# Performance work log

Hardware: AMD Instinct MI355X
Metric: run time of the kernel (lower is better)

The kernel has to match this reference:

```python
import jax, jax.numpy as jnp
import numpy as np

B, S, D = 2, 2048, 1024
H = 16
DH = D // H
FF = 4096
N_NEU = 4096
N_PAT = 64
K = 16          # neuron top-k
KP = 8          # pattern top-k
EPS = 1e-5


def _layer_norm(x, g, b):
    mu = jnp.mean(x, axis=-1, keepdims=True)
    var = jnp.mean((x - mu) ** 2, axis=-1, keepdims=True)
    return (x - mu) * jax.lax.rsqrt(var + EPS) * g + b


def setup_inputs() -> dict:
    key = jax.random.key(0)
    ks = jax.random.split(key, 20)
    sc = 0.02
    lin = lambda k, o, i: jax.random.normal(k, (o, i), jnp.float32) * (1.0 / np.sqrt(i))
    return {
        "x": jax.random.normal(ks[0], (B, S, D), jnp.float32),
        "neurons": jax.random.normal(ks[1], (N_NEU, D), jnp.float32) * sc,
        "wq": lin(ks[2], D, D), "bq": jnp.zeros((D,), jnp.float32),
        "wk": lin(ks[3], D, D), "bk": jnp.zeros((D,), jnp.float32),
        "wv": lin(ks[4], D, D), "bv": jnp.zeros((D,), jnp.float32),
        "wp": lin(ks[5], 2, 2 * D), "bp": jnp.zeros((2,), jnp.float32),
        "pattern_queries": jax.random.normal(ks[6], (N_PAT, D), jnp.float32) * sc,
        "gates": jax.random.normal(ks[7], (N_PAT, FF), jnp.float32) * sc,
        "w_up": lin(ks[8], FF, D), "b_up": jnp.zeros((FF,), jnp.float32),
        "w_down": lin(ks[9], D, FF), "b_down": jnp.zeros((D,), jnp.float32),
        "ln1_g": jnp.ones((D,), jnp.float32), "ln1_b": jnp.zeros((D,), jnp.float32),
        "ln2_g": jnp.ones((D,), jnp.float32), "ln2_b": jnp.zeros((D,), jnp.float32),
    }


def _forward(x, neurons, wq, bq, wk, bk, wv, bv, wp, bp, pattern_queries, gates,
             w_up, b_up, w_down, b_down, ln1_g, ln1_b, ln2_g, ln2_b):
    # ---- NeuronRouter on norm1(x) ----
    normed = _layer_norm(x, ln1_g, ln1_b)
    q = (normed @ wq.T + bq).reshape(B, S, H, DH).transpose(0, 2, 1, 3)
    k = (normed @ wk.T + bk).reshape(B, S, H, DH).transpose(0, 2, 1, 3)
    v = (normed @ wv.T + bv).reshape(B, S, H, DH).transpose(0, 2, 1, 3)
    attn = jax.nn.softmax(jnp.einsum('bhqd,bhkd->bhqk', q, k) / np.sqrt(DH), axis=-1)
    context = jnp.einsum('bhqk,bhkd->bhqd', attn, v).transpose(0, 2, 1, 3).reshape(B, S, D)

    token_scores = normed @ neurons.T                     # [B,S,N]
    context_scores = context @ neurons.T                  # [B,S,N]
    combined = jnp.concatenate([normed, context], axis=-1)
    path_w = jax.nn.softmax(combined @ wp.T + bp, axis=-1)  # [B,S,2]
    scores = path_w[..., 0:1] * token_scores + path_w[..., 1:2] * context_scores

    topk_scores, topk_idx = jax.lax.top_k(scores, K)      # [B,S,K]
    topk_weights = jax.nn.softmax(topk_scores, axis=-1)
    selected = neurons[topk_idx]                          # [B,S,K,D]
    router_out = jnp.einsum('bsk,bskd->bsd', topk_weights, selected)

    x = x + router_out

    # ---- PatternFFN on norm2(x) ----
    normed2 = _layer_norm(x, ln2_g, ln2_b)
    # similarity * neuron weight, summed over K -> pattern scores [B,S,P]
    pattern_scores = jnp.einsum('pd,bskd,bsk->bsp', pattern_queries, selected,
                                topk_weights) / np.sqrt(D)
    pat_scores, pat_idx = jax.lax.top_k(pattern_scores, KP)  # [B,S,KP]
    pat_weights = jax.nn.softmax(pat_scores, axis=-1)
    selected_gates = gates[pat_idx]                       # [B,S,KP,FF]
    ffn_gate = jnp.einsum('bsk,bskf->bsf', pat_weights, selected_gates)

    h = normed2 @ w_up.T + b_up                           # [B,S,FF]
    h = jax.nn.gelu(h * jax.nn.sigmoid(ffn_gate), approximate=False)
    ffn_out = h @ w_down.T + b_down

    return x + ffn_out, topk_idx


def reference(x, neurons, wq, bq, wk, bk, wv, bv, wp, bp, pattern_queries, gates,
              w_up, b_up, w_down, b_down, ln1_g, ln1_b, ln2_g, ln2_b):
    return _forward(x, neurons, wq, bq, wk, bk, wv, bv, wp, bp, pattern_queries,
                    gates, w_up, b_up, w_down, b_down, ln1_g, ln1_b, ln2_g, ln2_b)
```

## Files before the change

### kernel.cpp

```cpp
#include <hip/hip_runtime.h>
#include <math.h>

#define DEV static __device__ __forceinline__

constexpr int S_ = 2048;
constexpr int D_ = 1024;
constexpr int H_ = 16;

typedef __attribute__((ext_vector_type(8))) short bf16x8;
typedef __attribute__((ext_vector_type(4))) float f32x4;
typedef __attribute__((ext_vector_type(8))) short s16x8;

DEV unsigned short f2bf(float x) {
    union { float f; unsigned u; } c; c.f = x;
    const unsigned r = (c.u + 0x7FFFu + ((c.u >> 16) & 1u)) >> 16;
    return (unsigned short)r;
}
DEV float bf2f(unsigned short u) {
    union { unsigned u; float f; } c; c.u = ((unsigned)u) << 16;
    return c.f;
}

DEV float blockReduceSum(float v) {
    #pragma unroll
    for (int m = 1; m < 64; m <<= 1) v += __shfl_xor(v, m, 64);
    __shared__ float wsr[4];
    const int lane = threadIdx.x & 63, wid = threadIdx.x >> 6;
    if (lane == 0) wsr[wid] = v;
    __syncthreads();
    v = wsr[0] + wsr[1] + wsr[2] + wsr[3];
    __syncthreads();
    return v;
}

template<int BF16OUT>
__global__ __launch_bounds__(256)
void ln_k(const float* __restrict__ x, const float* __restrict__ g,
          const float* __restrict__ b, void* __restrict__ o)
{
    const int m = blockIdx.x, tid = threadIdx.x;
    const float* xr = x + (size_t)m * D_;
    const float4 xv = *(const float4*)(xr + tid * 4);
    float s = xv.x + xv.y + xv.z + xv.w;
    s = blockReduceSum(s);
    const float mu = s * (1.0f / 1024.0f);
    const float d0 = xv.x - mu, d1 = xv.y - mu, d2 = xv.z - mu, d3 = xv.w - mu;
    float sq = d0 * d0 + d1 * d1 + d2 * d2 + d3 * d3;
    sq = blockReduceSum(sq);
    const float rstd = rsqrtf(sq * (1.0f / 1024.0f) + 1e-5f);
    const float4 gv = *(const float4*)(g + tid * 4);
    const float4 bv = *(const float4*)(b + tid * 4);
    const float o0 = d0 * rstd * gv.x + bv.x;
    const float o1 = d1 * rstd * gv.y + bv.y;
    const float o2 = d2 * rstd * gv.z + bv.z;
    const float o3 = d3 * rstd * gv.w + bv.w;
    if constexpr (BF16OUT) {
        unsigned short* ob = (unsigned short*)o + (size_t)m * D_ + tid * 4;
        *(ushort4*)ob = make_ushort4(f2bf(o0), f2bf(o1), f2bf(o2), f2bf(o3));
    } else {
        *(float4*)((float*)o + (size_t)m * D_ + tid * 4) = make_float4(o0, o1, o2, o3);
    }
}

template<int MODE>
__global__ __launch_bounds__(256)
void gemm32_k(const float* __restrict__ A, const float* __restrict__ Bw,
              const float* __restrict__ bias, const float* __restrict__ extra,
              float* __restrict__ Cout, int M, int N, int Kd)
{
    __shared__ __align__(16) float As[32][132];
    __shared__ __align__(16) float Bs[32][132];
    const int tid = threadIdx.x;
    const int tx = tid & 15, ty = tid >> 4;
    const int row0 = blockIdx.y * 128, col0 = blockIdx.x * 128;
    const int lr = tid & 127, lk = (tid >> 7) * 16;
    const float* Ap = A + (size_t)(row0 + lr) * Kd + lk;
    const float* Bp = Bw + (size_t)(col0 + lr) * Kd + lk;
    float acc[8][8] = {};

    float4 ar[4], br[4];
    #pragma unroll
    for (int jj = 0; jj < 4; ++jj) {
        ar[jj] = *(const float4*)(Ap + jj * 4);
        br[jj] = *(const float4*)(Bp + jj * 4);
    }

    for (int k0 = 0; k0 < Kd; k0 += 32) {
        __syncthreads();
        #pragma unroll
        for (int jj = 0; jj < 4; ++jj) {
            As[lk + jj * 4 + 0][lr] = ar[jj].x;
            As[lk + jj * 4 + 1][lr] = ar[jj].y;
            As[lk + jj * 4 + 2][lr] = ar[jj].z;
            As[lk + jj * 4 + 3][lr] = ar[jj].w;
            Bs[lk + jj * 4 + 0][lr] = br[jj].x;
            Bs[lk + jj * 4 + 1][lr] = br[jj].y;
            Bs[lk + jj * 4 + 2][lr] = br[jj].z;
            Bs[lk + jj * 4 + 3][lr] = br[jj].w;
        }
        __syncthreads();
        if (k0 + 32 < Kd) {
            #pragma unroll
            for (int jj = 0; jj < 4; ++jj) {
                ar[jj] = *(const float4*)(Ap + k0 + 32 + jj * 4);
                br[jj] = *(const float4*)(Bp + k0 + 32 + jj * 4);
            }
        }
        #pragma unroll
        for (int kk = 0; kk < 32; ++kk) {
            float av[8], bv[8];
            *(float4*)&av[0] = *(const float4*)&As[kk][ty * 8];
            *(float4*)&av[4] = *(const float4*)&As[kk][ty * 8 + 4];
            *(float4*)&bv[0] = *(const float4*)&Bs[kk][tx * 8];
            *(float4*)&bv[4] = *(const float4*)&Bs[kk][tx * 8 + 4];
            #pragma unroll
            for (int r = 0; r < 8; ++r)
                #pragma unroll
                for (int c = 0; c < 8; ++c)
                    acc[r][c] = fmaf(av[r], bv[c], acc[r][c]);
        }
    }

    const int gr0 = row0 + ty * 8, gc0 = col0 + tx * 8;
    if constexpr (MODE == 0) {
        const int hh = gc0 >> 6, dh = gc0 & 63;
        const float4 bias0 = *(const float4*)(bias + gc0);
        const float4 bias1 = *(const float4*)(bias + gc0 + 4);
        #pragma unroll
        for (int r = 0; r < 8; ++r) {
            const int m = gr0 + r;
            const int bb = m >> 11, s = m & (S_ - 1);
            float* dst = Cout + (((size_t)(bb * H_ + hh) * S_ + s) * 64 + dh);
            *(float4*)dst = make_float4(acc[r][0] + bias0.x, acc[r][1] + bias0.y,
                                        acc[r][2] + bias0.z, acc[r][3] + bias0.w);
            *(float4*)(dst + 4) = make_float4(acc[r][4] + bias1.x, acc[r][5] + bias1.y,
                                              acc[r][6] + bias1.z, acc[r][7] + bias1.w);
        }
    } else if constexpr (MODE == 2) {
        #pragma unroll
        for (int r = 0; r < 8; ++r) {
            const float rs = extra[2 * (gr0 + r)];
            float* dst = Cout + (size_t)(gr0 + r) * N + gc0;
            *(float4*)dst = make_float4(rs * acc[r][0], rs * acc[r][1],
                                        rs * acc[r][2], rs * acc[r][3]);
            *(float4*)(dst + 4) = make_float4(rs * acc[r][4], rs * acc[r][5],
                                              rs * acc[r][6], rs * acc[r][7]);
        }
    } else if constexpr (MODE == 3) {
        #pragma unroll
        for (int r = 0; r < 8; ++r) {
            const float rs = extra[2 * (gr0 + r)];
            float* dst = Cout + (size_t)(gr0 + r) * N + gc0;
            const float4 c0 = *(const float4*)dst;
            const float4 c1 = *(const float4*)(dst + 4);
            *(float4*)dst = make_float4(c0.x + rs * acc[r][0], c0.y + rs * acc[r][1],
                                        c0.z + rs * acc[r][2], c0.w + rs * acc[r][3]);
            *(float4*)(dst + 4) = make_float4(c1.x + rs * acc[r][4], c1.y + rs * acc[r][5],
                                              c1.z + rs * acc[r][6], c1.w + rs * acc[r][7]);
        }
    }
}

__global__ __launch_bounds__(256)
void attn4_k(const float* __restrict__ q, const float* __restrict__ k,
             const float* __restrict__ v, float* __restrict__ ctx)
{
    __shared__ __align__(16) float Qs[64][68];
    __shared__ __align__(16) float KP[64][68];
    __shared__ __align__(16) float Vs[64][68];
    const int tid = threadIdx.x;
    const int tx = tid & 15, ty = tid >> 4;
    const int bh = blockIdx.y;
    const int q0 = blockIdx.x * 64;
    const float* qb = q + (size_t)bh * S_ * 64;
    const float* kb = k + (size_t)bh * S_ * 64;
    const float* vb = v + (size_t)bh * S_ * 64;

    const int j = tid & 63, dc = (tid >> 6) * 16;

    {
        const float* src = qb + (size_t)(q0 + j) * 64 + dc;
        const float4 t0 = *(const float4*)(src + 0);
        const float4 t1 = *(const float4*)(src + 4);
        const float4 t2 = *(const float4*)(src + 8);
        const float4 t3 = *(const float4*)(src + 12);
        Qs[dc + 0][j] = t0.x;  Qs[dc + 1][j] = t0.y;  Qs[dc + 2][j] = t0.z;  Qs[dc + 3][j] = t0.w;
        Qs[dc + 4][j] = t1.x;  Qs[dc + 5][j] = t1.y;  Qs[dc + 6][j] = t1.z;  Qs[dc + 7][j] = t1.w;
        Qs[dc + 8][j] = t2.x;  Qs[dc + 9][j] = t2.y;  Qs[dc + 10][j] = t2.z; Qs[dc + 11][j] = t2.w;
        Qs[dc + 12][j] = t3.x; Qs[dc + 13][j] = t3.y; Qs[dc + 14][j] = t3.z; Qs[dc + 15][j] = t3.w;
    }

    float4 kr0, kr1, kr2, kr3, vr0, vr1, vr2, vr3;
    {
        const float* ks = kb + (size_t)j * 64 + dc;
        const float* vs = vb + (size_t)j * 64 + dc;
        kr0 = *(const float4*)(ks + 0);  kr1 = *(const float4*)(ks + 4);
        kr2 = *(const float4*)(ks + 8);  kr3 = *(const float4*)(ks + 12);
        vr0 = *(const float4*)(vs + 0);  vr1 = *(const float4*)(vs + 4);
        vr2 = *(const float4*)(vs + 8);  vr3 = *(const float4*)(vs + 12);
    }

    float mrow[4] = {-INFINITY, -INFINITY, -INFINITY, -INFINITY};
    float lrow[4] = {0.f, 0.f, 0.f, 0.f};
    float acc[4][4] = {};

    for (int kt = 0; kt < S_; kt += 64) {
        __syncthreads();
        KP[dc + 0][j] = kr0.x;  KP[dc + 1][j] = kr0.y;  KP[dc + 2][j] = kr0.z;  KP[dc + 3][j] = kr0.w;
        KP[dc + 4][j] = kr1.x;  KP[dc + 5][j] = kr1.y;  KP[dc + 6][j] = kr1.z;  KP[dc + 7][j] = kr1.w;
        KP[dc + 8][j] = kr2.x;  KP[dc + 9][j] = kr2.y;  KP[dc + 10][j] = kr2.z; KP[dc + 11][j] = kr2.w;
        KP[dc + 12][j] = kr3.x; KP[dc + 13][j] = kr3.y; KP[dc + 14][j] = kr3.z; KP[dc + 15][j] = kr3.w;
        *(float4*)&Vs[j][dc + 0]  = vr0;
        *(float4*)&Vs[j][dc + 4]  = vr1;
        *(float4*)&Vs[j][dc + 8]  = vr2;
        *(float4*)&Vs[j][dc + 12] = vr3;
        __syncthreads();

        if (kt + 64 < S_) {
            const float* ks = kb + (size_t)(kt + 64 + j) * 64 + dc;
            const float* vs = vb + (size_t)(kt + 64 + j) * 64 + dc;
            kr0 = *(const float4*)(ks + 0);  kr1 = *(const float4*)(ks + 4);
            kr2 = *(const float4*)(ks + 8);  kr3 = *(const float4*)(ks + 12);
            vr0 = *(const float4*)(vs + 0);  vr1 = *(const float4*)(vs + 4);
            vr2 = *(const float4*)(vs + 8);  vr3 = *(const float4*)(vs + 12);
        }

        float s[4][4] = {};
        #pragma unroll 8
        for (int d = 0; d < 64; ++d) {
            const float4 q4 = *(const float4*)&Qs[d][ty * 4];
            const float4 k4 = *(const float4*)&KP[d][tx * 4];
            s[0][0] = fmaf(q4.x, k4.x, s[0][0]); s[0][1] = fmaf(q4.x, k4.y, s[0][1]);
            s[0][2] = fmaf(q4.x, k4.z, s[0][2]); s[0][3] = fmaf(q4.x, k4.w, s[0][3]);
            s[1][0] = fmaf(q4.y, k4.x, s[1][0]); s[1][1] = fmaf(q4.y, k4.y, s[1][1]);
            s[1][2] = fmaf(q4.y, k4.z, s[1][2]); s[1][3] = fmaf(q4.y, k4.w, s[1][3]);
            s[2][0] = fmaf(q4.z, k4.x, s[2][0]); s[2][1] = fmaf(q4.z, k4.y, s[2][1]);
            s[2][2] = fmaf(q4.z, k4.z, s[2][2]); s[2][3] = fmaf(q4.z, k4.w, s[2][3]);
            s[3][0] = fmaf(q4.w, k4.x, s[3][0]); s[3][1] = fmaf(q4.w, k4.y, s[3][1]);
            s[3][2] = fmaf(q4.w, k4.z, s[3][2]); s[3][3] = fmaf(q4.w, k4.w, s[3][3]);
        }

        float4 prow[4];
        #pragma unroll
        for (int r = 0; r < 4; ++r) {
            float s0 = s[r][0] * 0.125f, s1 = s[r][1] * 0.125f;
            float s2 = s[r][2] * 0.125f, s3 = s[r][3] * 0.125f;
            float rm = fmaxf(fmaxf(s0, s1), fmaxf(s2, s3));
            #pragma unroll
            for (int sh = 1; sh < 16; sh <<= 1) rm = fmaxf(rm, __shfl_xor(rm, sh, 64));
            const float mn = fmaxf(mrow[r], rm);
            const float p0 = expf(s0 - mn), p1 = expf(s1 - mn);
            const float p2 = expf(s2 - mn), p3 = expf(s3 - mn);
            float rs = p0 + p1 + p2 + p3;
            #pragma unroll
            for (int sh = 1; sh < 16; sh <<= 1) rs += __shfl_xor(rs, sh, 64);
            const float esc = expf(mrow[r] - mn);
            lrow[r] = lrow[r] * esc + rs;
            mrow[r] = mn;
            acc[r][0] *= esc; acc[r][1] *= esc; acc[r][2] *= esc; acc[r][3] *= esc;
            prow[r] = make_float4(p0, p1, p2, p3);
        }
        __syncthreads();
        #pragma unroll
        for (int r = 0; r < 4; ++r)
            *(float4*)&KP[ty * 4 + r][tx * 4] = prow[r];
        __syncthreads();

        #pragma unroll 4
        for (int jb = 0; jb < 16; ++jb) {
            const float4 v0 = *(const float4*)&Vs[jb * 4 + 0][tx * 4];
            const float4 v1 = *(const float4*)&Vs[jb * 4 + 1][tx * 4];
            const float4 v2 = *(const float4*)&Vs[jb * 4 + 2][tx * 4];
            const float4 v3 = *(const float4*)&Vs[jb * 4 + 3][tx * 4];
            #pragma unroll
            for (int r = 0; r < 4; ++r) {
                const float4 p4 = *(const float4*)&KP[ty * 4 + r][jb * 4];
                acc[r][0] = fmaf(p4.x, v0.x, acc[r][0]); acc[r][1] = fmaf(p4.x, v0.y, acc[r][1]);
                acc[r][2] = fmaf(p4.x, v0.z, acc[r][2]); acc[r][3] = fmaf(p4.x, v0.w, acc[r][3]);
                acc[r][0] = fmaf(p4.y, v1.x, acc[r][0]); acc[r][1] = fmaf(p4.y, v1.y, acc[r][1]);
                acc[r][2] = fmaf(p4.y, v1.z, acc[r][2]); acc[r][3] = fmaf(p4.y, v1.w, acc[r][3]);
                acc[r][0] = fmaf(p4.z, v2.x, acc[r][0]); acc[r][1] = fmaf(p4.z, v2.y, acc[r][1]);
                acc[r][2] = fmaf(p4.z, v2.z, acc[r][2]); acc[r][3] = fmaf(p4.z, v2.w, acc[r][3]);
                acc[r][0] = fmaf(p4.w, v3.x, acc[r][0]); acc[r][1] = fmaf(p4.w, v3.y, acc[r][1]);
                acc[r][2] = fmaf(p4.w, v3.z, acc[r][2]); acc[r][3] = fmaf(p4.w, v3.w, acc[r][3]);
            }
        }
    }

    const int bb = bh >> 4, hh = bh & 15;
    #pragma unroll
    for (int r = 0; r < 4; ++r) {
        const float inv = 1.0f / lrow[r];
        *(float4*)(ctx + (size_t)(bb * S_ + q0 + ty * 4 + r) * D_ + hh * 64 + tx * 4) =
            make_float4(acc[r][0] * inv, acc[r][1] * inv, acc[r][2] * inv, acc[r][3] * inv);
    }
}

__global__ __launch_bounds__(256)
void pathw_k(const float* __restrict__ normed, const float* __restrict__ ctx,
             const float* __restrict__ wp, const float* __restrict__ bp,
             float* __restrict__ pw)
{
    const int m = blockIdx.x, tid = threadIdx.x;
    const float4 n4 = *(const float4*)(normed + (size_t)m * D_ + tid * 4);
    const float4 c4 = *(const float4*)(ctx + (size_t)m * D_ + tid * 4);
    const float4 w0n = *(const float4*)(wp + tid * 4);
    const float4 w0c = *(const float4*)(wp + 1024 + tid * 4);
    const float4 w1n = *(const float4*)(wp + 2048 + tid * 4);
    const float4 w1c = *(const float4*)(wp + 3072 + tid * 4);
    float p0 = n4.x * w0n.x + n4.y * w0n.y + n4.z * w0n.z + n4.w * w0n.w
             + c4.x * w0c.x + c4.y * w0c.y + c4.z * w0c.z + c4.w * w0c.w;
    float p1 = n4.x * w1n.x + n4.y * w1n.y + n4.z * w1n.z + n4.w * w1n.w
             + c4.x * w1c.x + c4.y * w1c.y + c4.z * w1c.z + c4.w * w1c.w;
    p0 = blockReduceSum(p0);
    p1 = blockReduceSum(p1);
    if (tid == 0) {
        const float l0 = p0 + bp[0], l1 = p1 + bp[1];
        const float mx = fmaxf(l0, l1);
        const float e0 = expf(l0 - mx), e1 = expf(l1 - mx);
        const float inv = 1.0f / (e0 + e1);
        pw[2 * m] = e0 * inv;
        pw[2 * m + 1] = e1 * inv;
    }
}

__global__ __launch_bounds__(256)
void topk_router_k(const float* __restrict__ scores, const float* __restrict__ neurons,
                   const float* __restrict__ x, float* __restrict__ idx_out,
                   float* __restrict__ x1, float* __restrict__ router)
{
    __shared__ __align__(16) float sc[4096];
    __shared__ unsigned long long wred[4];
    __shared__ int ki_s[16];
    __shared__ float kv_s[16];
    __shared__ float kw_s[16];
    const int m = blockIdx.x, tid = threadIdx.x;
    const float* srow = scores + (size_t)m * 4096;
    for (int i = tid; i < 1024; i += 256)
        *(float4*)&sc[i * 4] = *(const float4*)(srow + i * 4);
    __syncthreads();

    for (int t = 0; t < 16; ++t) {
        unsigned long long best = 0ull;
        for (int i = tid; i < 4096; i += 256) {
            unsigned u = __float_as_uint(sc[i]);
            u = (u & 0x80000000u) ? ~u : (u | 0x80000000u);
            const unsigned long long key =
                ((unsigned long long)u << 32) | (unsigned long long)(0xFFFFFFFFu - (unsigned)i);
            if (key > best) best = key;
        }
        #pragma unroll
        for (int sh = 1; sh < 64; sh <<= 1) {
            const unsigned long long o = __shfl_xor(best, sh, 64);
            if (o > best) best = o;
        }
        if ((tid & 63) == 0) wred[tid >> 6] = best;
        __syncthreads();
        if (tid == 0) {
            unsigned long long bb = wred[0];
            if (wred[1] > bb) bb = wred[1];
            if (wred[2] > bb) bb = wred[2];
            if (wred[3] > bb) bb = wred[3];
            const int idx = (int)(0xFFFFFFFFu - (unsigned)(bb & 0xFFFFFFFFull));
            ki_s[t] = idx;
            kv_s[t] = sc[idx];
            sc[idx] = -INFINITY;
        }
        __syncthreads();
    }

    if (tid == 0) {
        const float mx = kv_s[0];
        float es[16], sum = 0.f;
        #pragma unroll
        for (int t = 0; t < 16; ++t) { es[t] = expf(kv_s[t] - mx); sum += es[t]; }
        const float inv = 1.0f / sum;
        #pragma unroll
        for (int t = 0; t < 16; ++t) kw_s[t] = es[t] * inv;
    }
    __syncthreads();

    if (tid < 16) idx_out[(size_t)m * 16 + tid] = (float)ki_s[tid];

    float4 r = make_float4(0.f, 0.f, 0.f, 0.f);
    #pragma unroll
    for (int t = 0; t < 16; ++t) {
        const float w = kw_s[t];
        const float4 nv = *(const float4*)(neurons + (size_t)ki_s[t] * D_ + tid * 4);
        r.x = fmaf(w, nv.x, r.x); r.y = fmaf(w, nv.y, r.y);
        r.z = fmaf(w, nv.z, r.z); r.w = fmaf(w, nv.w, r.w);
    }
    const float4 xv = *(const float4*)(x + (size_t)m * D_ + tid * 4);
    *(float4*)(router + (size_t)m * D_ + tid * 4) = r;
    *(float4*)(x1 + (size_t)m * D_ + tid * 4) =
        make_float4(xv.x + r.x, xv.y + r.y, xv.z + r.z, xv.w + r.w);
}

__global__ __launch_bounds__(256)
void pattern_k(const float* __restrict__ router, const float* __restrict__ pq,
               const float* __restrict__ gates, unsigned short* __restrict__ gate_out)
{
    __shared__ __align__(16) float rr[1024];
    __shared__ float ps[64];
    __shared__ int pidx[8];
    __shared__ float pwt[8];
    const int m = blockIdx.x, tid = threadIdx.x;
    *(float4*)&rr[tid * 4] = *(const float4*)(router + (size_t)m * D_ + tid * 4);
    __syncthreads();

    const int p = tid >> 2, part = tid & 3;
    const float* pqr = pq + (size_t)p * D_ + part * 256;
    float sum = 0.f;
    for (int d = 0; d < 256; d += 4) {
        const float4 a = *(const float4*)(pqr + d);
        const float4 b = *(const float4*)&rr[part * 256 + d];
        sum += a.x * b.x + a.y * b.y + a.z * b.z + a.w * b.w;
    }
    sum += __shfl_xor(sum, 1, 64);
    sum += __shfl_xor(sum, 2, 64);
    if (part == 0) ps[p] = sum * (1.0f / 32.0f);
    __syncthreads();

    if (tid == 0) {
        float kv[8];
        for (int t = 0; t < 8; ++t) {
            float bv = -INFINITY; int bi = 0;
            for (int i = 0; i < 64; ++i) {
                const float vv = ps[i];
                if (vv > bv) { bv = vv; bi = i; }
            }
            kv[t] = bv; pidx[t] = bi; ps[bi] = -INFINITY;
        }
        const float mx = kv[0];
        float ee[8], tot = 0.f;
        for (int t = 0; t < 8; ++t) { ee[t] = expf(kv[t] - mx); tot += ee[t]; }
        for (int t = 0; t < 8; ++t) pwt[t] = ee[t] / tot;
    }
    __syncthreads();

    for (int f = tid * 4; f < 4096; f += 1024) {
        float4 g = make_float4(0.f, 0.f, 0.f, 0.f);
        #pragma unroll
        for (int t = 0; t < 8; ++t) {
            const float w = pwt[t];
            const float4 gv = *(const float4*)(gates + (size_t)pidx[t] * 4096 + f);
            g.x = fmaf(w, gv.x, g.x); g.y = fmaf(w, gv.y, g.y);
            g.z = fmaf(w, gv.z, g.z); g.w = fmaf(w, gv.w, g.w);
        }
        *(ushort4*)(gate_out + (size_t)m * 4096 + f) =
            make_ushort4(f2bf(g.x), f2bf(g.y), f2bf(g.z), f2bf(g.w));
    }
}

__global__ __launch_bounds__(256)
void castbf_k(const float* __restrict__ in, unsigned short* __restrict__ out, int n)
{
    const int i = (blockIdx.x * 256 + threadIdx.x) * 8;
    if (i >= n) return;
    const float4 a = *(const float4*)(in + i);
    const float4 b = *(const float4*)(in + i + 4);
    *(ushort4*)(out + i) = make_ushort4(f2bf(a.x), f2bf(a.y), f2bf(a.z), f2bf(a.w));
    *(ushort4*)(out + i + 4) = make_ushort4(f2bf(b.x), f2bf(b.y), f2bf(b.z), f2bf(b.w));
}

template<int EPI>
__global__ __launch_bounds__(256)
void gemmbf_k(const unsigned short* __restrict__ A, const unsigned short* __restrict__ Bw,
              const float* __restrict__ bias, const unsigned short* __restrict__ gate,
              const float* resid, void* Cout, int M, int N, int Kd)
{
    constexpr int LSH = 40;
    __shared__ __align__(16) unsigned short Al[128 * LSH];
    __shared__ __align__(16) unsigned short Bl[128 * LSH];
    const int tid = threadIdx.x;
    const int lane = tid & 63;
    const int w = tid >> 6, wr = w >> 1, wc = w & 1;
    const int row0 = blockIdx.y * 128, col0 = blockIdx.x * 128;

    const int o0 = tid * 16, o1 = o0 + 4096;
    const int r0 = o0 >> 6, k0e = (o0 & 63) >> 1;
    const int r1 = o1 >> 6, k1e = (o1 & 63) >> 1;
    const int l0 = r0 * LSH + k0e, l1 = r1 * LSH + k1e;
    const unsigned short* Ap0 = A + (size_t)(row0 + r0) * Kd + k0e;
    const unsigned short* Ap1 = A + (size_t)(row0 + r1) * Kd + k1e;
    const unsigned short* Bp0 = Bw + (size_t)(col0 + r0) * Kd + k0e;
    const unsigned short* Bp1 = Bw + (size_t)(col0 + r1) * Kd + k1e;

    f32x4 acc[4][4];
    #pragma unroll
    for (int m = 0; m < 4; ++m)
        #pragma unroll
        for (int n = 0; n < 4; ++n)
            #pragma unroll
            for (int e = 0; e < 4; ++e) acc[m][n][e] = 0.f;

    s16x8 ra0 = *(const s16x8*)Ap0;
    s16x8 ra1 = *(const s16x8*)Ap1;
    s16x8 rb0 = *(const s16x8*)Bp0;
    s16x8 rb1 = *(const s16x8*)Bp1;

    const int fr = lane & 15, kg = (lane >> 4) * 8;
    const unsigned short* aBase = Al + ((wr * 64 + fr) * LSH + kg);
    const unsigned short* bBase = Bl + ((wc * 64 + fr) * LSH + kg);

    for (int k0 = 0; k0 < Kd; k0 += 32) {
        __syncthreads();
        *(s16x8*)(Al + l0) = ra0;
        *(s16x8*)(Al + l1) = ra1;
        *(s16x8*)(Bl + l0) = rb0;
        *(s16x8*)(Bl + l1) = rb1;
        __syncthreads();
        if (k0 + 32 < Kd) {
            ra0 = *(const s16x8*)(Ap0 + k0 + 32);
            ra1 = *(const s16x8*)(Ap1 + k0 + 32);
            rb0 = *(const s16x8*)(Bp0 + k0 + 32);
            rb1 = *(const s16x8*)(Bp1 + k0 + 32);
        }
        bf16x8 aF[4], bF[4];
        #pragma unroll
        for (int m = 0; m < 4; ++m) aF[m] = *(const bf16x8*)(aBase + m * 16 * LSH);
        #pragma unroll
        for (int n = 0; n < 4; ++n) bF[n] = *(const bf16x8*)(bBase + n * 16 * LSH);
        #pragma unroll
        for (int m = 0; m < 4; ++m)
            #pragma unroll
            for (int n = 0; n < 4; ++n)
                acc[m][n] = __builtin_amdgcn_mfma_f32_16x16x32_bf16(aF[m], bF[n], acc[m][n], 0, 0, 0);
    }

    const int rbase = (lane >> 4) * 4;
    #pragma unroll
    for (int m = 0; m < 4; ++m) {
        #pragma unroll
        for (int n = 0; n < 4; ++n) {
            const int gcol = col0 + wc * 64 + n * 16 + (lane & 15);
            const int growb = row0 + wr * 64 + m * 16 + rbase;
            const float bc = bias[gcol];
            #pragma unroll
            for (int r = 0; r < 4; ++r) {
                const int grow = growb + r;
                const float vv = acc[m][n][r];
                if constexpr (EPI == 0) {
                    const float z = vv + bc;
                    const float gt = bf2f(gate[(size_t)grow * N + gcol]);
                    const float zz = z / (1.f + expf(-gt));
                    const float o = 0.5f * zz * (1.f + erff(zz * 0.70710678118654752440f));
                    ((unsigned short*)Cout)[(size_t)grow * N + gcol] = f2bf(o);
                } else {
                    ((float*)Cout)[(size_t)grow * N + gcol] =
                        vv + bc + resid[(size_t)grow * N + gcol];
                }
            }
        }
    }
}

extern "C" void kernel_launch(void* const* d_in, const int* in_sizes, int n_in,
                              void* d_out, int out_size, void* d_ws, size_t ws_size,
                              hipStream_t stream)
{
    const float* x      = (const float*)d_in[0];
    const float* neurons= (const float*)d_in[1];
    const float* wq = (const float*)d_in[2];  const float* bq = (const float*)d_in[3];
    const float* wk = (const float*)d_in[4];  const float* bk = (const float*)d_in[5];
    const float* wv = (const float*)d_in[6];  const float* bv = (const float*)d_in[7];
    const float* wp = (const float*)d_in[8];  const float* bp = (const float*)d_in[9];
    const float* pq = (const float*)d_in[10];
    const float* gates = (const float*)d_in[11];
    const float* w_up = (const float*)d_in[12];  const float* b_up = (const float*)d_in[13];
    const float* w_dn = (const float*)d_in[14];  const float* b_dn = (const float*)d_in[15];
    const float* ln1g = (const float*)d_in[16];  const float* ln1b = (const float*)d_in[17];
    const float* ln2g = (const float*)d_in[18];  const float* ln2b = (const float*)d_in[19];

    float* out0    = (float*)d_out;
    float* idx_out = out0 + (size_t)4096 * 1024;

    float* ws      = (float*)d_ws;
    float* scores  = ws;
    float* normed  = ws + 16777216;
    float* qb      = ws + 20971520;
    float* kb      = ws + 25165824;
    float* vb      = ws + 29360128;
    float* ctx     = ws + 33554432;
    float* router  = ws + 37748736;
    float* pw      = ws + 41943040;

    unsigned short* gate_bf   = (unsigned short*)qb;
    unsigned short* h_bf      = (unsigned short*)scores;
    unsigned short* normed2bf = (unsigned short*)(scores + 8388608);
    unsigned short* wup_bf    = (unsigned short*)router;
    unsigned short* wdn_bf    = wup_bf + 4194304;
    float* x1 = out0;

    const dim3 blk(256);

    ln_k<0><<<4096, blk, 0, stream>>>(x, ln1g, ln1b, normed);
    gemm32_k<0><<<dim3(8, 32), blk, 0, stream>>>(normed, wq, bq, nullptr, qb, 4096, 1024, 1024);
    gemm32_k<0><<<dim3(8, 32), blk, 0, stream>>>(normed, wk, bk, nullptr, kb, 4096, 1024, 1024);
    gemm32_k<0><<<dim3(8, 32), blk, 0, stream>>>(normed, wv, bv, nullptr, vb, 4096, 1024, 1024);
    attn4_k<<<dim3(32, 32), blk, 0, stream>>>(qb, kb, vb, ctx);
    pathw_k<<<4096, blk, 0, stream>>>(normed, ctx, wp, bp, pw);
    gemm32_k<2><<<dim3(32, 32), blk, 0, stream>>>(normed, neurons, nullptr, pw, scores, 4096, 4096, 1024);
    gemm32_k<3><<<dim3(32, 32), blk, 0, stream>>>(ctx, neurons, nullptr, pw + 1, scores, 4096, 4096, 1024);
    topk_router_k<<<4096, blk, 0, stream>>>(scores, neurons, x, idx_out, x1, router);
    ln_k<1><<<4096, blk, 0, stream>>>(x1, ln2g, ln2b, normed2bf);
    pattern_k<<<4096, blk, 0, stream>>>(router, pq, gates, gate_bf);
    castbf_k<<<2048, blk, 0, stream>>>(w_up, wup_bf, 4194304);
    castbf_k<<<2048, blk, 0, stream>>>(w_dn, wdn_bf, 4194304);
    gemmbf_k<0><<<dim3(32, 32), blk, 0, stream>>>(normed2bf, wup_bf, b_up, gate_bf, nullptr, h_bf, 4096, 4096, 1024);
    gemmbf_k<1><<<dim3(8, 32), blk, 0, stream>>>(h_bf, wdn_bf, b_dn, nullptr, x1, out0, 4096, 1024, 4096);
}
```

Measured before the change: 2.131 ms.

## Fuse QKV GEMMs, router tail kernels, weight casts, and add XCD block swizzle

Merges the three Q/K/V projection launches into one grid, and folds top-k routing, LayerNorm2 and the pattern scoring into a single per-row kernel so the router output never goes through global memory. The two weight casts become one launch. An XCD-aware block index swizzle is added to all GEMMs so neighbouring tiles land on the same chiplet and share its L2. The aim is to cut launch count and global round trips, at the cost of higher per-block shared memory and register use in the fused tail kernel.

```diff
diff --git a/kernel.cpp b/kernel.cpp
--- a/kernel.cpp
+++ b/kernel.cpp
@@ -21,6 +21,11 @@
     return c.f;
 }
 
+DEV int xcd_swizzle(int wg, int nwg) {
+    const int nx = nwg >> 3;
+    return (wg & 7) * nx + (wg >> 3);
+}
+
 DEV float blockReduceSum(float v) {
     #pragma unroll
     for (int m = 1; m < 64; m <<= 1) v += __shfl_xor(v, m, 64);
@@ -33,10 +38,9 @@
     return v;
 }
 
-template<int BF16OUT>
 __global__ __launch_bounds__(256)
 void ln_k(const float* __restrict__ x, const float* __restrict__ g,
-          const float* __restrict__ b, void* __restrict__ o)
+          const float* __restrict__ b, float* __restrict__ o)
 {
     const int m = blockIdx.x, tid = threadIdx.x;
     const float* xr = x + (size_t)m * D_;
@@ -50,29 +54,33 @@
     const float rstd = rsqrtf(sq * (1.0f / 1024.0f) + 1e-5f);
     const float4 gv = *(const float4*)(g + tid * 4);
     const float4 bv = *(const float4*)(b + tid * 4);
-    const float o0 = d0 * rstd * gv.x + bv.x;
-    const float o1 = d1 * rstd * gv.y + bv.y;
-    const float o2 = d2 * rstd * gv.z + bv.z;
-    const float o3 = d3 * rstd * gv.w + bv.w;
-    if constexpr (BF16OUT) {
-        unsigned short* ob = (unsigned short*)o + (size_t)m * D_ + tid * 4;
-        *(ushort4*)ob = make_ushort4(f2bf(o0), f2bf(o1), f2bf(o2), f2bf(o3));
-    } else {
-        *(float4*)((float*)o + (size_t)m * D_ + tid * 4) = make_float4(o0, o1, o2, o3);
-    }
-}
-
-template<int MODE>
-__global__ __launch_bounds__(256)
-void gemm32_k(const float* __restrict__ A, const float* __restrict__ Bw,
-              const float* __restrict__ bias, const float* __restrict__ extra,
-              float* __restrict__ Cout, int M, int N, int Kd)
-{
+    *(float4*)(o + (size_t)m * D_ + tid * 4) =
+        make_float4(d0 * rstd * gv.x + bv.x, d1 * rstd * gv.y + bv.y,
+                    d2 * rstd * gv.z + bv.z, d3 * rstd * gv.w + bv.w);
+}
+
+__global__ __launch_bounds__(256)
+void gemmqkv_k(const float* __restrict__ A,
+               const float* __restrict__ Bq, const float* __restrict__ Bk2,
+               const float* __restrict__ Bv,
+               const float* __restrict__ bq, const float* __restrict__ bk2,
+               const float* __restrict__ bv, float* __restrict__ Cout)
+{
+    const int Kd = 1024;
     __shared__ __align__(16) float As[32][132];
     __shared__ __align__(16) float Bs[32][132];
     const int tid = threadIdx.x;
     const int tx = tid & 15, ty = tid >> 4;
-    const int row0 = blockIdx.y * 128, col0 = blockIdx.x * 128;
+    const int swz = xcd_swizzle(blockIdx.y * gridDim.x + blockIdx.x,
+                                gridDim.x * gridDim.y);
+    const int bx = swz % gridDim.x, by = swz / gridDim.x;
+    const int row0 = by * 128, col0g = bx * 128;
+    const int which = col0g >> 10;
+    const float* Bw = (which == 0) ? Bq : ((which == 1) ? Bk2 : Bv);
+    const float* bias = (which == 0) ? bq : ((which == 1) ? bk2 : bv);
+    float* Cb = Cout + (size_t)which * 4194304;
+    const int col0 = col0g & 1023;
+
     const int lr = tid & 127, lk = (tid >> 7) * 16;
     const float* Ap = A + (size_t)(row0 + lr) * Kd + lk;
     const float* Bp = Bw + (size_t)(col0 + lr) * Kd + lk;
@@ -108,6 +116,84 @@
         }
         #pragma unroll
         for (int kk = 0; kk < 32; ++kk) {
+            float av[8], bv2[8];
+            *(float4*)&av[0] = *(const float4*)&As[kk][ty * 8];
+            *(float4*)&av[4] = *(const float4*)&As[kk][ty * 8 + 4];
+            *(float4*)&bv2[0] = *(const float4*)&Bs[kk][tx * 8];
+            *(float4*)&bv2[4] = *(const float4*)&Bs[kk][tx * 8 + 4];
+            #pragma unroll
+            for (int r = 0; r < 8; ++r)
+                #pragma unroll
+                for (int c = 0; c < 8; ++c)
+                    acc[r][c] = fmaf(av[r], bv2[c], acc[r][c]);
+        }
+    }
+
+    const int gr0 = row0 + ty * 8, gc0 = col0 + tx * 8;
+    const int hh = gc0 >> 6, dh = gc0 & 63;
+    const float4 bias0 = *(const float4*)(bias + gc0);
+    const float4 bias1 = *(const float4*)(bias + gc0 + 4);
+    #pragma unroll
+    for (int r = 0; r < 8; ++r) {
+        const int m = gr0 + r;
+        const int bb = m >> 11, s = m & (S_ - 1);
+        float* dst = Cb + (((size_t)(bb * H_ + hh) * S_ + s) * 64 + dh);
+        *(float4*)dst = make_float4(acc[r][0] + bias0.x, acc[r][1] + bias0.y,
+                                    acc[r][2] + bias0.z, acc[r][3] + bias0.w);
+        *(float4*)(dst + 4) = make_float4(acc[r][4] + bias1.x, acc[r][5] + bias1.y,
+                                          acc[r][6] + bias1.z, acc[r][7] + bias1.w);
+    }
+}
+
+template<int MODE>
+__global__ __launch_bounds__(256)
+void gemm32_k(const float* __restrict__ A, const float* __restrict__ Bw,
+              const float* __restrict__ bias, const float* __restrict__ extra,
+              float* __restrict__ Cout, int M, int N, int Kd)
+{
+    __shared__ __align__(16) float As[32][132];
+    __shared__ __align__(16) float Bs[32][132];
+    const int tid = threadIdx.x;
+    const int tx = tid & 15, ty = tid >> 4;
+    const int swz = xcd_swizzle(blockIdx.y * gridDim.x + blockIdx.x,
+                                gridDim.x * gridDim.y);
+    const int bx = swz % gridDim.x, by = swz / gridDim.x;
+    const int row0 = by * 128, col0 = bx * 128;
+    const int lr = tid & 127, lk = (tid >> 7) * 16;
+    const float* Ap = A + (size_t)(row0 + lr) * Kd + lk;
+    const float* Bp = Bw + (size_t)(col0 + lr) * Kd + lk;
+    float acc[8][8] = {};
+
+    float4 ar[4], br[4];
+    #pragma unroll
+    for (int jj = 0; jj < 4; ++jj) {
+        ar[jj] = *(const float4*)(Ap + jj * 4);
+        br[jj] = *(const float4*)(Bp + jj * 4);
+    }
+
+    for (int k0 = 0; k0 < Kd; k0 += 32) {
+        __syncthreads();
+        #pragma unroll
+        for (int jj = 0; jj < 4; ++jj) {
+            As[lk + jj * 4 + 0][lr] = ar[jj].x;
+            As[lk + jj * 4 + 1][lr] = ar[jj].y;
+            As[lk + jj * 4 + 2][lr] = ar[jj].z;
+            As[lk + jj * 4 + 3][lr] = ar[jj].w;
+            Bs[lk + jj * 4 + 0][lr] = br[jj].x;
+            Bs[lk + jj * 4 + 1][lr] = br[jj].y;
+            Bs[lk + jj * 4 + 2][lr] = br[jj].z;
+            Bs[lk + jj * 4 + 3][lr] = br[jj].w;
+        }
+        __syncthreads();
+        if (k0 + 32 < Kd) {
+            #pragma unroll
+            for (int jj = 0; jj < 4; ++jj) {
+                ar[jj] = *(const float4*)(Ap + k0 + 32 + jj * 4);
+                br[jj] = *(const float4*)(Bp + k0 + 32 + jj * 4);
+            }
+        }
+        #pragma unroll
+        for (int kk = 0; kk < 32; ++kk) {
             float av[8], bv[8];
             *(float4*)&av[0] = *(const float4*)&As[kk][ty * 8];
             *(float4*)&av[4] = *(const float4*)&As[kk][ty * 8 + 4];
@@ -122,21 +208,7 @@
     }
 
     const int gr0 = row0 + ty * 8, gc0 = col0 + tx * 8;
-    if constexpr (MODE == 0) {
-        const int hh = gc0 >> 6, dh = gc0 & 63;
-        const float4 bias0 = *(const float4*)(bias + gc0);
-        const float4 bias1 = *(const float4*)(bias + gc0 + 4);
-        #pragma unroll
-        for (int r = 0; r < 8; ++r) {
-            const int m = gr0 + r;
-            const int bb = m >> 11, s = m & (S_ - 1);
-            float* dst = Cout + (((size_t)(bb * H_ + hh) * S_ + s) * 64 + dh);
-            *(float4*)dst = make_float4(acc[r][0] + bias0.x, acc[r][1] + bias0.y,
-                                        acc[r][2] + bias0.z, acc[r][3] + bias0.w);
-            *(float4*)(dst + 4) = make_float4(acc[r][4] + bias1.x, acc[r][5] + bias1.y,
-                                              acc[r][6] + bias1.z, acc[r][7] + bias1.w);
-        }
-    } else if constexpr (MODE == 2) {
+    if constexpr (MODE == 2) {
         #pragma unroll
         for (int r = 0; r < 8; ++r) {
             const float rs = extra[2 * (gr0 + r)];
@@ -146,7 +218,7 @@
             *(float4*)(dst + 4) = make_float4(rs * acc[r][4], rs * acc[r][5],
                                               rs * acc[r][6], rs * acc[r][7]);
         }
-    } else if constexpr (MODE == 3) {
+    } else {
         #pragma unroll
         for (int r = 0; r < 8; ++r) {
             const float rs = extra[2 * (gr0 + r)];
@@ -325,15 +397,21 @@
 }
 
 __global__ __launch_bounds__(256)
-void topk_router_k(const float* __restrict__ scores, const float* __restrict__ neurons,
-                   const float* __restrict__ x, float* __restrict__ idx_out,
-                   float* __restrict__ x1, float* __restrict__ router)
+void router_tail_k(const float* __restrict__ scores, const float* __restrict__ neurons,
+                   const float* __restrict__ x, const float* __restrict__ ln2g,
+                   const float* __restrict__ ln2b, const float* __restrict__ pq,
+                   const float* __restrict__ gates, float* __restrict__ idx_out,
+                   float* __restrict__ x1, unsigned short* __restrict__ normed2bf,
+                   unsigned short* __restrict__ gate_out)
 {
     __shared__ __align__(16) float sc[4096];
     __shared__ unsigned long long wred[4];
     __shared__ int ki_s[16];
     __shared__ float kv_s[16];
     __shared__ float kw_s[16];
+    __shared__ float ps[64];
+    __shared__ int pidx[8];
+    __shared__ float pwt[8];
     const int m = blockIdx.x, tid = threadIdx.x;
     const float* srow = scores + (size_t)m * 4096;
     for (int i = tid; i < 1024; i += 256)
@@ -391,21 +469,28 @@
         r.z = fmaf(w, nv.z, r.z); r.w = fmaf(w, nv.w, r.w);
     }
     const float4 xv = *(const float4*)(x + (size_t)m * D_ + tid * 4);
-    *(float4*)(router + (size_t)m * D_ + tid * 4) = r;
-    *(float4*)(x1 + (size_t)m * D_ + tid * 4) =
-        make_float4(xv.x + r.x, xv.y + r.y, xv.z + r.z, xv.w + r.w);
-}
-
-__global__ __launch_bounds__(256)
-void pattern_k(const float* __restrict__ router, const float* __restrict__ pq,
-               const float* __restrict__ gates, unsigned short* __restrict__ gate_out)
-{
-    __shared__ __align__(16) float rr[1024];
-    __shared__ float ps[64];
-    __shared__ int pidx[8];
-    __shared__ float pwt[8];
-    const int m = blockIdx.x, tid = threadIdx.x;
-    *(float4*)&rr[tid * 4] = *(const float4*)(router + (size_t)m * D_ + tid * 4);
+    const float x0 = xv.x + r.x, x1v = xv.y + r.y, x2 = xv.z + r.z, x3 = xv.w + r.w;
+    *(float4*)(x1 + (size_t)m * D_ + tid * 4) = make_float4(x0, x1v, x2, x3);
+
+    {
+        float s = x0 + x1v + x2 + x3;
+        s = blockReduceSum(s);
+        const float mu = s * (1.0f / 1024.0f);
+        const float d0 = x0 - mu, d1 = x1v - mu, d2 = x2 - mu, d3 = x3 - mu;
+        float sq = d0 * d0 + d1 * d1 + d2 * d2 + d3 * d3;
+        sq = blockReduceSum(sq);
+        const float rstd = rsqrtf(sq * (1.0f / 1024.0f) + 1e-5f);
+        const float4 gv = *(const float4*)(ln2g + tid * 4);
+        const float4 bv = *(const float4*)(ln2b + tid * 4);
+        unsigned short* ob = normed2bf + (size_t)m * D_ + tid * 4;
+        *(ushort4*)ob = make_ushort4(f2bf(d0 * rstd * gv.x + bv.x),
+                                     f2bf(d1 * rstd * gv.y + bv.y),
+                                     f2bf(d2 * rstd * gv.z + bv.z),
+                                     f2bf(d3 * rstd * gv.w + bv.w));
+    }
+
+    __syncthreads();
+    *(float4*)&sc[tid * 4] = r;
     __syncthreads();
 
     const int p = tid >> 2, part = tid & 3;
@@ -413,7 +498,7 @@
     float sum = 0.f;
     for (int d = 0; d < 256; d += 4) {
         const float4 a = *(const float4*)(pqr + d);
-        const float4 b = *(const float4*)&rr[part * 256 + d];
+        const float4 b = *(const float4*)&sc[part * 256 + d];
         sum += a.x * b.x + a.y * b.y + a.z * b.z + a.w * b.w;
     }
     sum += __shfl_xor(sum, 1, 64);
@@ -453,14 +538,18 @@
 }
 
 __global__ __launch_bounds__(256)
-void castbf_k(const float* __restrict__ in, unsigned short* __restrict__ out, int n)
-{
-    const int i = (blockIdx.x * 256 + threadIdx.x) * 8;
-    if (i >= n) return;
-    const float4 a = *(const float4*)(in + i);
-    const float4 b = *(const float4*)(in + i + 4);
-    *(ushort4*)(out + i) = make_ushort4(f2bf(a.x), f2bf(a.y), f2bf(a.z), f2bf(a.w));
-    *(ushort4*)(out + i + 4) = make_ushort4(f2bf(b.x), f2bf(b.y), f2bf(b.z), f2bf(b.w));
+void castbf2_k(const float* __restrict__ a, const float* __restrict__ b,
+               unsigned short* __restrict__ oa, unsigned short* __restrict__ ob)
+{
+    int i = (blockIdx.x * 256 + threadIdx.x) * 8;
+    const float* src;
+    unsigned short* dst;
+    if (i < 4194304) { src = a + i; dst = oa + i; }
+    else { src = b + (i - 4194304); dst = ob + (i - 4194304); }
+    const float4 u = *(const float4*)(src);
+    const float4 v = *(const float4*)(src + 4);
+    *(ushort4*)(dst) = make_ushort4(f2bf(u.x), f2bf(u.y), f2bf(u.z), f2bf(u.w));
+    *(ushort4*)(dst + 4) = make_ushort4(f2bf(v.x), f2bf(v.y), f2bf(v.z), f2bf(v.w));
 }
 
 template<int EPI>
@@ -475,7 +564,9 @@
     const int tid = threadIdx.x;
     const int lane = tid & 63;
     const int w = tid >> 6, wr = w >> 1, wc = w & 1;
-    const int row0 = blockIdx.y * 128, col0 = blockIdx.x * 128;
+    const int swz = xcd_swizzle(blockIdx.y * gridDim.x + blockIdx.x,
+                                gridDim.x * gridDim.y);
+    const int row0 = (swz / gridDim.x) * 128, col0 = (swz % gridDim.x) * 128;
 
     const int o0 = tid * 16, o1 = o0 + 4096;
     const int r0 = o0 >> 6, k0e = (o0 & 63) >> 1;
@@ -586,27 +677,23 @@
     float* pw      = ws + 41943040;
 
     unsigned short* gate_bf   = (unsigned short*)qb;
+    unsigned short* normed2bf = (unsigned short*)vb;
     unsigned short* h_bf      = (unsigned short*)scores;
-    unsigned short* normed2bf = (unsigned short*)(scores + 8388608);
     unsigned short* wup_bf    = (unsigned short*)router;
     unsigned short* wdn_bf    = wup_bf + 4194304;
     float* x1 = out0;
 
     const dim3 blk(256);
 
-    ln_k<0><<<4096, blk, 0, stream>>>(x, ln1g, ln1b, normed);
-    gemm32_k<0><<<dim3(8, 32), blk, 0, stream>>>(normed, wq, bq, nullptr, qb, 4096, 1024, 1024);
-    gemm32_k<0><<<dim3(8, 32), blk, 0, stream>>>(normed, wk, bk, nullptr, kb, 4096, 1024, 1024);
-    gemm32_k<0><<<dim3(8, 32), blk, 0, stream>>>(normed, wv, bv, nullptr, vb, 4096, 1024, 1024);
+    ln_k<<<4096, blk, 0, stream>>>(x, ln1g, ln1b, normed);
+    gemmqkv_k<<<dim3(24, 32), blk, 0, stream>>>(normed, wq, wk, wv, bq, bk, bv, qb);
     attn4_k<<<dim3(32, 32), blk, 0, stream>>>(qb, kb, vb, ctx);
     pathw_k<<<4096, blk, 0, stream>>>(normed, ctx, wp, bp, pw);
     gemm32_k<2><<<dim3(32, 32), blk, 0, stream>>>(normed, neurons, nullptr, pw, scores, 4096, 4096, 1024);
     gemm32_k<3><<<dim3(32, 32), blk, 0, stream>>>(ctx, neurons, nullptr, pw + 1, scores, 4096, 4096, 1024);
-    topk_router_k<<<4096, blk, 0, stream>>>(scores, neurons, x, idx_out, x1, router);
-    ln_k<1><<<4096, blk, 0, stream>>>(x1, ln2g, ln2b, normed2bf);
-    pattern_k<<<4096, blk, 0, stream>>>(router, pq, gates, gate_bf);
-    castbf_k<<<2048, blk, 0, stream>>>(w_up, wup_bf, 4194304);
-    castbf_k<<<2048, blk, 0, stream>>>(w_dn, wdn_bf, 4194304);
+    router_tail_k<<<4096, blk, 0, stream>>>(scores, neurons, x, ln2g, ln2b, pq, gates,
+                                            idx_out, x1, normed2bf, gate_bf);
+    castbf2_k<<<4096, blk, 0, stream>>>(w_up, w_dn, wup_bf, wdn_bf);
     gemmbf_k<0><<<dim3(32, 32), blk, 0, stream>>>(normed2bf, wup_bf, b_up, gate_bf, nullptr, h_bf, 4096, 4096, 1024);
     gemmbf_k<1><<<dim3(8, 32), blk, 0, stream>>>(h_bf, wdn_bf, b_dn, nullptr, x1, out0, 4096, 1024, 4096);
 }
```

New measurement: 2.024 ms, median of 2. 5.0% less time.
